# Optimization experiments

Measured on AMD Instinct MI355X. Metric: run time of the kernel, lower is better.

The kernel has to match this reference:

```python
import jax, jax.numpy as jnp
import numpy as np

E = 1024   # embed_dim
H = 16     # num_heads
R = 256    # rank
HD = E // H
B, S = 2, 2048


def setup_inputs() -> dict:
    key = jax.random.key(0)
    ks = jax.random.split(key, 20)
    sc = 0.02
    d = {
        'query': jax.random.normal(ks[0], (B, S, E), jnp.float32),
        'key':   jax.random.normal(ks[1], (B, S, E), jnp.float32),
        'value': jax.random.normal(ks[2], (B, S, E), jnp.float32),
    }
    names = ['q', 'k', 'v', 'o']
    i = 3
    for n in names:
        d[f'W{n}_lo'] = jax.random.normal(ks[i], (E, R), jnp.float32) * sc; i += 1
        d[f'b{n}_lo'] = jnp.zeros((R,), jnp.float32)
        d[f'W{n}_hi'] = jax.random.normal(ks[i], (R, E), jnp.float32) * sc; i += 1
        d[f'b{n}_hi'] = jnp.zeros((E,), jnp.float32)
    return d


def _lowrank(x, W_lo, b_lo, W_hi, b_hi):
    # Linear(E->R) then Linear(R->E)
    return (x @ W_lo + b_lo) @ W_hi + b_hi


def reference(query, key, value,
              Wq_lo, bq_lo, Wq_hi, bq_hi,
              Wk_lo, bk_lo, Wk_hi, bk_hi,
              Wv_lo, bv_lo, Wv_hi, bv_hi,
              Wo_lo, bo_lo, Wo_hi, bo_hi):
    b, s, _ = query.shape
    q = _lowrank(query, Wq_lo, bq_lo, Wq_hi, bq_hi)
    k = _lowrank(key,   Wk_lo, bk_lo, Wk_hi, bk_hi)
    v = _lowrank(value, Wv_lo, bv_lo, Wv_hi, bv_hi)
    # (B, S, E) -> (B, H, S, HD)
    q = q.reshape(b, s, H, HD).transpose(0, 2, 1, 3)
    k = k.reshape(b, s, H, HD).transpose(0, 2, 1, 3)
    v = v.reshape(b, s, H, HD).transpose(0, 2, 1, 3)
    scores = jnp.einsum('bhqd,bhkd->bhqk', q, k) / jnp.sqrt(jnp.float32(HD))
    attn = jax.nn.softmax(scores, axis=-1)  # dropout p=0.0 -> identity
    out = jnp.einsum('bhqk,bhkd->bhqd', attn, v)
    out = out.transpose(0, 2, 1, 3).reshape(b, s, E)
    return _lowrank(out, Wo_lo, bo_lo, Wo_hi, bo_hi)
```

## Files before the change

kernel.cpp:

```cpp
#include <hip/hip_runtime.h>

namespace {

constexpr int kE  = 1024;
constexpr int kH  = 16;
constexpr int kR  = 256;
constexpr int kHD = 64;
constexpr int kB  = 2;
constexpr int kS  = 2048;
constexpr int kM  = kB * kS;

typedef float  floatx4 __attribute__((ext_vector_type(4)));
typedef short  short8  __attribute__((ext_vector_type(8)));
typedef short  short4  __attribute__((ext_vector_type(4)));
typedef unsigned int uint2v __attribute__((ext_vector_type(2)));

__device__ inline short f2bf(float f) {
  union { float f; unsigned u; } x{f};
  unsigned r = x.u + 0x7FFF + ((x.u >> 16) & 1);
  return (short)(r >> 16);
}

__device__ inline unsigned cvt_pk_bf16(float a, float b) {
#if defined(__HIP_DEVICE_COMPILE__)
  unsigned r;
  asm("v_cvt_pk_bf16_f32 %0, %1, %2" : "=v"(r) : "v"(a), "v"(b));
  return r;
#else
  return (unsigned)(unsigned short)f2bf(a) | ((unsigned)(unsigned short)f2bf(b) << 16);
#endif
}

__device__ inline short4 pack2(unsigned a, unsigned b) {
  union { uint2v u; short4 s; } x;
  x.u[0] = a; x.u[1] = b;
  return x.s;
}

__device__ inline short8 pack4(unsigned a, unsigned b, unsigned c, unsigned d) {
  union { unsigned u[4]; short8 s; } x;
  x.u[0] = a; x.u[1] = b; x.u[2] = c; x.u[3] = d;
  return x.s;
}

__device__ inline float fexp2(float x) {
#if defined(__HIP_DEVICE_COMPILE__) && __has_builtin(__builtin_amdgcn_exp2f)
  return __builtin_amdgcn_exp2f(x);
#else
  return exp2f(x);
#endif
}

__device__ inline int xcd_swz256(int bid) {
  return ((bid & 7) << 5) | (bid >> 3);
}

#if defined(__HIP_DEVICE_COMPILE__)
  #if __has_builtin(__builtin_amdgcn_mfma_f32_16x16x16bf16_1k)
    #define MFMA16(a, b, c) __builtin_amdgcn_mfma_f32_16x16x16bf16_1k(a, b, c, 0, 0, 0)
  #elif __has_builtin(__builtin_amdgcn_mfma_f32_16x16x16_bf16)
    #define MFMA16(a, b, c) __builtin_amdgcn_mfma_f32_16x16x16_bf16(a, b, c, 0, 0, 0)
  #else
    #error "no 16x16x16 bf16 MFMA builtin on device"
  #endif
#else
  #define MFMA16(a, b, c) (c)
#endif

struct PrepArgs { const float* src[8]; short* dst[8]; };

__global__ __launch_bounds__(256) void prep_weights(PrepArgs pa) {
  const int id = blockIdx.y;
  const bool lo = (id & 1) == 0;
  const int K = lo ? 1024 : 256;
  const int N = lo ? 256 : 1024;
  const int tiles_k = K >> 6;
  const int k0 = (blockIdx.x % tiles_k) * 64;
  const int n0 = (blockIdx.x / tiles_k) * 64;
  const float* src = pa.src[id];
  short* dst = pa.dst[id];

  __shared__ float tile[64][68];
  const int t  = threadIdx.x;
  const int c4 = (t & 15) * 4;
  const int r  = t >> 4;

#pragma unroll
  for (int i = 0; i < 4; ++i) {
    const int rk = r + i * 16;
    *(float4*)&tile[rk][c4] = *(const float4*)&src[(size_t)(k0 + rk) * N + n0 + c4];
  }
  __syncthreads();
#pragma unroll
  for (int i = 0; i < 4; ++i) {
    const int rn = r + i * 16;
    short4 o = { f2bf(tile[c4 + 0][rn]), f2bf(tile[c4 + 1][rn]),
                 f2bf(tile[c4 + 2][rn]), f2bf(tile[c4 + 3][rn]) };
    *(short4*)&dst[(size_t)(n0 + rn) * K + k0 + c4] = o;
  }
}

struct GemmArgs {
  const short* A[3]; const short* Bt[3]; const float* bias[3];
  void* C[3]; float scale[3];
};

template <int M, int N, int K, int BM, int BN, int MODE>
__global__ __launch_bounds__(256) void gemm_bf16(GemmArgs args) {
  constexpr int TILES_N = N / BN;
  constexpr int WTM = BM / 2, WTN = BN / 2;
  constexpr int FI = WTM / 16, FJ = WTN / 16;
  constexpr int AROUNDS = (BM * 64) / 4096;
  constexpr int BROUNDS = (BN * 64) / 4096;
  constexpr int P = 80;
  static_assert((M / BM) * (N / BN) == 256, "swizzle assumes nwg=256");
  static_assert(MODE != 1 || M == kM, "MODE1 decode assumes M=4096");

  const int z = blockIdx.y;
  const int swz = xcd_swz256(blockIdx.x);
  const int row0 = (swz / TILES_N) * BM;
  const int col0 = (swz % TILES_N) * BN;
  const short* A  = args.A[z];
  const short* Bt = args.Bt[z];
  const float* bias = args.bias[z];
  const float scale = args.scale[z];

  __shared__ short As[BM * 40];
  __shared__ short Bs[BN * 40];

  const int t    = threadIdx.x;
  const int wave = t >> 6;
  const int lane = t & 63;
  const int lq   = lane & 15;
  const int quad = lane >> 4;
  const int wm0  = (wave >> 1) * WTM;
  const int wn0  = (wave & 1) * WTN;

  const int srow = t >> 2;
  const int scol = (t & 3) * 8;
  const int sbyte = (t & 3) * 16;

  floatx4 acc[FI][FJ] = {};

  short8 ra[AROUNDS], rb[BROUNDS];
#pragma unroll
  for (int r = 0; r < AROUNDS; ++r)
    ra[r] = *(const short8*)(A + (size_t)(row0 + r * 64 + srow) * K + scol);
#pragma unroll
  for (int r = 0; r < BROUNDS; ++r)
    rb[r] = *(const short8*)(Bt + (size_t)(col0 + r * 64 + srow) * K + scol);

  for (int kk = 0; kk < K; kk += 32) {
    __syncthreads();
#pragma unroll
    for (int r = 0; r < AROUNDS; ++r)
      *(short8*)((char*)As + (r * 64 + srow) * P + sbyte) = ra[r];
#pragma unroll
    for (int r = 0; r < BROUNDS; ++r)
      *(short8*)((char*)Bs + (r * 64 + srow) * P + sbyte) = rb[r];
    __syncthreads();

    if (kk + 32 < K) {
#pragma unroll
      for (int r = 0; r < AROUNDS; ++r)
        ra[r] = *(const short8*)(A + (size_t)(row0 + r * 64 + srow) * K + kk + 32 + scol);
#pragma unroll
      for (int r = 0; r < BROUNDS; ++r)
        rb[r] = *(const short8*)(Bt + (size_t)(col0 + r * 64 + srow) * K + kk + 32 + scol);
    }

    short8 af[FI], bf[FJ];
#pragma unroll
    for (int i = 0; i < FI; ++i)
      af[i] = *(const short8*)((const char*)As + ((wm0 + i * 16 + lq) * P + quad * 16));
#pragma unroll
    for (int j = 0; j < FJ; ++j)
      bf[j] = *(const short8*)((const char*)Bs + ((wn0 + j * 16 + lq) * P + quad * 16));
#pragma unroll
    for (int i = 0; i < FI; ++i)
#pragma unroll
      for (int j = 0; j < FJ; ++j)
        acc[i][j] = __builtin_amdgcn_mfma_f32_16x16x32_bf16(af[i], bf[j], acc[i][j], 0, 0, 0);
  }

#pragma unroll
  for (int i = 0; i < FI; ++i) {
    const int rbase = row0 + wm0 + i * 16 + quad * 4;
#pragma unroll
    for (int j = 0; j < FJ; ++j) {
      const int col = col0 + wn0 + j * 16 + lq;
      const float bj = bias[col];
      if (MODE == 2) {
        float* C = (float*)args.C[z];
#pragma unroll
        for (int r = 0; r < 4; ++r)
          C[(size_t)(rbase + r) * N + col] = (acc[i][j][r] + bj) * scale;
      } else if (MODE == 1) {
        short* C = (short*)args.C[z];
        const int h = col >> 6, d = col & 63;
        const int b = rbase >> 11, s = rbase & 2047;
        if (z == 2) {
          short4 o = { f2bf(acc[i][j][0] + bj), f2bf(acc[i][j][1] + bj),
                       f2bf(acc[i][j][2] + bj), f2bf(acc[i][j][3] + bj) };
          *(short4*)&C[((size_t)((b * 16 + h) * 64 + d)) * 2048 + s] = o;
        } else {
#pragma unroll
          for (int r = 0; r < 4; ++r)
            C[((size_t)((b * 16 + h) * 2048 + s + r)) * 64 + d] =
                f2bf((acc[i][j][r] + bj) * scale);
        }
      } else {
        short* C = (short*)args.C[z];
#pragma unroll
        for (int r = 0; r < 4; ++r)
          C[(size_t)(rbase + r) * N + col] = f2bf((acc[i][j][r] + bj) * scale);
      }
    }
  }
}

struct GemmLoArgs {
  const float* A[3]; const short* Bt[3]; const float* bias[3]; short* C[3];
};

__global__ __launch_bounds__(256) void gemm_lo_f32a(GemmLoArgs args) {
  constexpr int N = kR, K = kE, BM = 64, BN = 64;
  constexpr int TILES_N = N / BN;
  constexpr int WTM = BM / 2, WTN = BN / 2;
  constexpr int FI = WTM / 16, FJ = WTN / 16;
  constexpr int P = 80;
  static_assert((kM / BM) * (N / BN) == 256, "swizzle assumes nwg=256");

  const int z = blockIdx.y;
  const int swz = xcd_swz256(blockIdx.x);
  const int row0 = (swz / TILES_N) * BM;
  const int col0 = (swz % TILES_N) * BN;
  const float* A  = args.A[z];
  const short* Bt = args.Bt[z];
  const float* bias = args.bias[z];
  short* C = args.C[z];

  __shared__ float As32[64][36];
  __shared__ short Bs[BN * 40];

  const int t    = threadIdx.x;
  const int wave = t >> 6;
  const int lane = t & 63;
  const int lq   = lane & 15;
  const int quad = lane >> 4;
  const int wm0  = (wave >> 1) * WTM;
  const int wn0  = (wave & 1) * WTN;

  const int arow  = t >> 2;
  const int acolf = (t & 3) * 8;
  const int srow  = t >> 2;
  const int scol  = (t & 3) * 8;
  const int sbyte = (t & 3) * 16;

  floatx4 acc[FI][FJ] = {};

  const float* arow_p = A + (size_t)(row0 + arow) * K + acolf;
  float4 ga0 = *(const float4*)(arow_p);
  float4 ga1 = *(const float4*)(arow_p + 4);
  short8 rb  = *(const short8*)(Bt + (size_t)(col0 + srow) * K + scol);

  for (int kk = 0; kk < K; kk += 32) {
    __syncthreads();
    *(float4*)&As32[arow][acolf]     = ga0;
    *(float4*)&As32[arow][acolf + 4] = ga1;
    *(short8*)((char*)Bs + srow * P + sbyte) = rb;
    __syncthreads();

    if (kk + 32 < K) {
      ga0 = *(const float4*)(arow_p + kk + 32);
      ga1 = *(const float4*)(arow_p + kk + 36);
      rb  = *(const short8*)(Bt + (size_t)(col0 + srow) * K + kk + 32 + scol);
    }

    short8 af[FI], bf[FJ];
#pragma unroll
    for (int i = 0; i < FI; ++i) {
      const int r = wm0 + i * 16 + lq;
      float4 f0 = *(const float4*)&As32[r][quad * 8];
      float4 f1 = *(const float4*)&As32[r][quad * 8 + 4];
      af[i] = pack4(cvt_pk_bf16(f0.x, f0.y), cvt_pk_bf16(f0.z, f0.w),
                    cvt_pk_bf16(f1.x, f1.y), cvt_pk_bf16(f1.z, f1.w));
    }
#pragma unroll
    for (int j = 0; j < FJ; ++j)
      bf[j] = *(const short8*)((const char*)Bs + ((wn0 + j * 16 + lq) * P + quad * 16));
#pragma unroll
    for (int i = 0; i < FI; ++i)
#pragma unroll
      for (int j = 0; j < FJ; ++j)
        acc[i][j] = __builtin_amdgcn_mfma_f32_16x16x32_bf16(af[i], bf[j], acc[i][j], 0, 0, 0);
  }

#pragma unroll
  for (int i = 0; i < FI; ++i) {
    const int rbase = row0 + wm0 + i * 16 + quad * 4;
#pragma unroll
    for (int j = 0; j < FJ; ++j) {
      const int col = col0 + wn0 + j * 16 + lq;
      const float bj = bias[col];
#pragma unroll
      for (int r = 0; r < 4; ++r)
        C[(size_t)(rbase + r) * N + col] = f2bf(acc[i][j][r] + bj);
    }
  }
}

__global__ __launch_bounds__(256) void attn_mfma(
    const short* __restrict__ Qp, const short* __restrict__ Kp,
    const short* __restrict__ Vtp, short* __restrict__ O)
{
  __shared__ short Ks[64][72];
  __shared__ short Vs[64][72];

  const int t    = threadIdx.x;
  const int wave = t >> 6;
  const int lane = t & 63;
  const int lq   = lane & 15;
  const int quad = lane >> 4;

  const int q0 = blockIdx.x * 128;
  const int bh = blockIdx.y;
  const int b  = bh >> 4;
  const int h  = bh & 15;

  short8 qf0[2], qf1[2];
#pragma unroll
  for (int qt = 0; qt < 2; ++qt) {
    const short* qrow = Qp + ((size_t)bh * kS + q0 + wave * 32 + qt * 16 + lq) * 64;
    qf0[qt] = *(const short8*)(qrow + quad * 8);
    qf1[qt] = *(const short8*)(qrow + 32 + quad * 8);
  }

  const short* Kbase = Kp  + (size_t)bh * kS * 64;
  const short* Vbase = Vtp + (size_t)bh * 64 * kS;

  const int srow = wave * 16 + (lane >> 3);
  const int scol = (lane & 7) * 8;

  floatx4 Oacc[4][2] = {};
  float m[2] = {-1e30f, -1e30f};
  float l[2] = {0.f, 0.f};

  short8 gk0 = *(const short8*)(Kbase + (size_t)(srow) * 64 + scol);
  short8 gk1 = *(const short8*)(Kbase + (size_t)(srow + 8) * 64 + scol);
  short8 gv0 = *(const short8*)(Vbase + (size_t)srow * kS + scol);
  short8 gv1 = *(const short8*)(Vbase + (size_t)(srow + 8) * kS + scol);

  for (int kc = 0; kc < kS; kc += 64) {
    __syncthreads();
    *(short8*)&Ks[srow][scol]     = gk0;
    *(short8*)&Ks[srow + 8][scol] = gk1;
    *(short8*)&Vs[srow][scol]     = gv0;
    *(short8*)&Vs[srow + 8][scol] = gv1;
    __syncthreads();

    if (kc + 64 < kS) {
      gk0 = *(const short8*)(Kbase + (size_t)(kc + 64 + srow) * 64 + scol);
      gk1 = *(const short8*)(Kbase + (size_t)(kc + 64 + srow + 8) * 64 + scol);
      gv0 = *(const short8*)(Vbase + (size_t)srow * kS + kc + 64 + scol);
      gv1 = *(const short8*)(Vbase + (size_t)(srow + 8) * kS + kc + 64 + scol);
    }

    floatx4 Sc[4][2];
#pragma unroll
    for (int tt = 0; tt < 4; ++tt) {
      short8 a0 = *(const short8*)&Ks[tt * 16 + lq][quad * 8];
      short8 a1 = *(const short8*)&Ks[tt * 16 + lq][32 + quad * 8];
#pragma unroll
      for (int qt = 0; qt < 2; ++qt) {
        floatx4 c = {};
        c = __builtin_amdgcn_mfma_f32_16x16x32_bf16(a0, qf0[qt], c, 0, 0, 0);
        c = __builtin_amdgcn_mfma_f32_16x16x32_bf16(a1, qf1[qt], c, 0, 0, 0);
        Sc[tt][qt] = c;
      }
    }

    short4 pf[4][2];
#pragma unroll
    for (int qt = 0; qt < 2; ++qt) {
      float x0 = fmaxf(fmaxf(Sc[0][qt][0], Sc[0][qt][1]), fmaxf(Sc[0][qt][2], Sc[0][qt][3]));
      float x1 = fmaxf(fmaxf(Sc[1][qt][0], Sc[1][qt][1]), fmaxf(Sc[1][qt][2], Sc[1][qt][3]));
      float x2 = fmaxf(fmaxf(Sc[2][qt][0], Sc[2][qt][1]), fmaxf(Sc[2][qt][2], Sc[2][qt][3]));
      float x3 = fmaxf(fmaxf(Sc[3][qt][0], Sc[3][qt][1]), fmaxf(Sc[3][qt][2], Sc[3][qt][3]));
      float plane = fmaxf(fmaxf(x0, x1), fmaxf(x2, x3));

      if (!__all(plane <= m[qt] + 10.f)) {
        float mc = fmaxf(plane, __shfl_xor(plane, 16, 64));
        mc = fmaxf(mc, __shfl_xor(mc, 32, 64));
        const float mn = fmaxf(m[qt], mc);
        const float a = fexp2(m[qt] - mn);
        m[qt] = mn;
        l[qt] *= a;
#pragma unroll
        for (int dt = 0; dt < 4; ++dt) Oacc[dt][qt] *= a;
      }

      float ls = 0.f;
#pragma unroll
      for (int tt = 0; tt < 4; ++tt) {
        float p0 = fexp2(Sc[tt][qt][0] - m[qt]);
        float p1 = fexp2(Sc[tt][qt][1] - m[qt]);
        float p2 = fexp2(Sc[tt][qt][2] - m[qt]);
        float p3 = fexp2(Sc[tt][qt][3] - m[qt]);
        ls += (p0 + p1) + (p2 + p3);
        pf[tt][qt] = pack2(cvt_pk_bf16(p0, p1), cvt_pk_bf16(p2, p3));
      }
      l[qt] += ls;
    }

#pragma unroll
    for (int dt = 0; dt < 4; ++dt) {
#pragma unroll
      for (int tt = 0; tt < 4; ++tt) {
        short4 vf = *(const short4*)&Vs[dt * 16 + lq][tt * 16 + quad * 4];
#pragma unroll
        for (int qt = 0; qt < 2; ++qt)
          Oacc[dt][qt] = MFMA16(vf, pf[tt][qt], Oacc[dt][qt]);
      }
    }
  }

#pragma unroll
  for (int qt = 0; qt < 2; ++qt) {
    float lv = l[qt];
    lv += __shfl_xor(lv, 16, 64);
    lv += __shfl_xor(lv, 32, 64);
    const float inv = 1.f / lv;

    short* orow = O + ((size_t)(b * kS + q0 + wave * 32 + qt * 16 + lq)) * kE + h * kHD;
#pragma unroll
    for (int dt = 0; dt < 4; ++dt) {
      short4 o = pack2(cvt_pk_bf16(Oacc[dt][qt][0] * inv, Oacc[dt][qt][1] * inv),
                       cvt_pk_bf16(Oacc[dt][qt][2] * inv, Oacc[dt][qt][3] * inv));
      *(short4*)&orow[dt * 16 + quad * 4] = o;
    }
  }
}

}

extern "C" void kernel_launch(void* const* d_in, const int* in_sizes, int n_in,
                              void* d_out, int out_size, void* d_ws, size_t ws_size,
                              hipStream_t stream) {
  short* ws = (short*)d_ws;
  short* Tq  = ws;
  short* Tk  = Tq  + (size_t)kM * kR;
  short* Tv  = Tk  + (size_t)kM * kR;
  short* Qh  = Tv  + (size_t)kM * kR;
  short* Kh  = Qh  + (size_t)kM * kE;
  short* Vth = Kh  + (size_t)kM * kE;
  short* Ab  = Vth + (size_t)kM * kE;
  short* To  = Ab  + (size_t)kM * kE;
  short* Wt  = To  + (size_t)kM * kR;

  short* WtArr[8];
  for (int i = 0; i < 8; ++i) WtArr[i] = Wt + (size_t)i * (kE * kR);

  PrepArgs pa;
  const int widx[8] = {3, 5, 7, 9, 11, 13, 15, 17};
  for (int i = 0; i < 8; ++i) { pa.src[i] = (const float*)d_in[widx[i]]; pa.dst[i] = WtArr[i]; }
  prep_weights<<<dim3(64, 8), dim3(256), 0, stream>>>(pa);

  {
    GemmLoArgs ga;
    ga.A[0] = (const float*)d_in[0]; ga.A[1] = (const float*)d_in[1]; ga.A[2] = (const float*)d_in[2];
    ga.Bt[0] = WtArr[0]; ga.Bt[1] = WtArr[2]; ga.Bt[2] = WtArr[4];
    ga.bias[0] = (const float*)d_in[4]; ga.bias[1] = (const float*)d_in[8]; ga.bias[2] = (const float*)d_in[12];
    ga.C[0] = Tq; ga.C[1] = Tk; ga.C[2] = Tv;
    gemm_lo_f32a<<<dim3(256, 3), dim3(256), 0, stream>>>(ga);
  }

  {
    GemmArgs ga;
    ga.A[0] = Tq; ga.A[1] = Tk; ga.A[2] = Tv;
    ga.Bt[0] = WtArr[1]; ga.Bt[1] = WtArr[3]; ga.Bt[2] = WtArr[5];
    ga.bias[0] = (const float*)d_in[6]; ga.bias[1] = (const float*)d_in[10]; ga.bias[2] = (const float*)d_in[14];
    ga.C[0] = Qh; ga.C[1] = Kh; ga.C[2] = Vth;
    ga.scale[0] = 0.125f * 1.44269504088896340736f;
    ga.scale[1] = 1.f; ga.scale[2] = 1.f;
    gemm_bf16<kM, kE, kR, 128, 128, 1><<<dim3(256, 3), dim3(256), 0, stream>>>(ga);
  }

  attn_mfma<<<dim3(kS / 128, kB * kH), dim3(256), 0, stream>>>(Qh, Kh, Vth, Ab);

  {
    GemmArgs ga;
    ga.A[0] = Ab; ga.Bt[0] = WtArr[6];
    ga.bias[0] = (const float*)d_in[16];
    ga.C[0] = To; ga.scale[0] = 1.f;
    gemm_bf16<kM, kR, kE, 64, 64, 0><<<dim3(256, 1), dim3(256), 0, stream>>>(ga);
  }
  {
    GemmArgs ga;
    ga.A[0] = To; ga.Bt[0] = WtArr[7];
    ga.bias[0] = (const float*)d_in[18];
    ga.C[0] = d_out; ga.scale[0] = 1.f;
    gemm_bf16<kM, kE, kR, 128, 128, 2><<<dim3(256, 1), dim3(256), 0, stream>>>(ga);
  }
}
```

Before: 243.8 us.

## Fuse output low-rank projections into one kernel keeping intermediate in LDS

Replaces the two output-projection GEMM launches with a single kernel. Each block computes a 64x256 low-rank intermediate from the attention output, keeps it in shared memory as bf16, then multiplies by the high-rank weight for its 256-column slice. This removes one launch and the global round trip of the intermediate. The cost is that the first GEMM is recomputed by each of the four column blocks that share a row tile.

```diff
diff --git a/kernel.cpp b/kernel.cpp
--- a/kernel.cpp
+++ b/kernel.cpp
@@ -310,6 +310,134 @@
   }
 }
 
+__global__ __launch_bounds__(256) void gemm_out_fused(
+    const short* __restrict__ Ab,
+    const short* __restrict__ BtLo,
+    const short* __restrict__ BtHi,
+    const float* __restrict__ bLo,
+    const float* __restrict__ bHi,
+    float* __restrict__ Out)
+{
+  constexpr int P  = 80;
+  constexpr int PT = 264;
+
+  const int swz = xcd_swz256(blockIdx.x);
+  const int r0 = (swz >> 2) * 64;
+  const int c0 = (swz & 3) * 256;
+
+  __shared__ short As[64 * 40];
+  __shared__ short Bs[256 * 40];
+  __shared__ short To[64 * PT];
+
+  const int t    = threadIdx.x;
+  const int wave = t >> 6;
+  const int lane = t & 63;
+  const int lq   = lane & 15;
+  const int quad = lane >> 4;
+  const int wm0  = (wave >> 1) * 32;
+  const int wn0  = (wave & 1) * 128;
+
+  const int srow  = t >> 2;
+  const int scol  = (t & 3) * 8;
+  const int sbyte = (t & 3) * 16;
+
+  floatx4 acc[2][8] = {};
+
+  short8 ra = *(const short8*)(Ab + (size_t)(r0 + srow) * 1024 + scol);
+  short8 rb[4];
+#pragma unroll
+  for (int r = 0; r < 4; ++r)
+    rb[r] = *(const short8*)(BtLo + (size_t)(r * 64 + srow) * 1024 + scol);
+
+  for (int kk = 0; kk < 1024; kk += 32) {
+    __syncthreads();
+    *(short8*)((char*)As + srow * P + sbyte) = ra;
+#pragma unroll
+    for (int r = 0; r < 4; ++r)
+      *(short8*)((char*)Bs + (r * 64 + srow) * P + sbyte) = rb[r];
+    __syncthreads();
+
+    if (kk + 32 < 1024) {
+      ra = *(const short8*)(Ab + (size_t)(r0 + srow) * 1024 + kk + 32 + scol);
+#pragma unroll
+      for (int r = 0; r < 4; ++r)
+        rb[r] = *(const short8*)(BtLo + (size_t)(r * 64 + srow) * 1024 + kk + 32 + scol);
+    }
+
+    short8 af[2], bf[8];
+#pragma unroll
+    for (int i = 0; i < 2; ++i)
+      af[i] = *(const short8*)((const char*)As + ((wm0 + i * 16 + lq) * P + quad * 16));
+#pragma unroll
+    for (int j = 0; j < 8; ++j)
+      bf[j] = *(const short8*)((const char*)Bs + ((wn0 + j * 16 + lq) * P + quad * 16));
+#pragma unroll
+    for (int i = 0; i < 2; ++i)
+#pragma unroll
+      for (int j = 0; j < 8; ++j)
+        acc[i][j] = __builtin_amdgcn_mfma_f32_16x16x32_bf16(af[i], bf[j], acc[i][j], 0, 0, 0);
+  }
+
+  short8 rb2[4];
+#pragma unroll
+  for (int r = 0; r < 4; ++r)
+    rb2[r] = *(const short8*)(BtHi + (size_t)(c0 + r * 64 + srow) * 256 + scol);
+
+#pragma unroll
+  for (int i = 0; i < 2; ++i) {
+    const int rbase = wm0 + i * 16 + quad * 4;
+#pragma unroll
+    for (int j = 0; j < 8; ++j) {
+      const int col = wn0 + j * 16 + lq;
+      const float bj = bLo[col];
+#pragma unroll
+      for (int r = 0; r < 4; ++r)
+        To[(rbase + r) * PT + col] = f2bf(acc[i][j][r] + bj);
+    }
+  }
+
+  floatx4 acc2[2][8] = {};
+  for (int kk = 0; kk < 256; kk += 32) {
+    __syncthreads();
+#pragma unroll
+    for (int r = 0; r < 4; ++r)
+      *(short8*)((char*)Bs + (r * 64 + srow) * P + sbyte) = rb2[r];
+    __syncthreads();
+
+    if (kk + 32 < 256) {
+#pragma unroll
+      for (int r = 0; r < 4; ++r)
+        rb2[r] = *(const short8*)(BtHi + (size_t)(c0 + r * 64 + srow) * 256 + kk + 32 + scol);
+    }
+
+    short8 af[2], bf[8];
+#pragma unroll
+    for (int i = 0; i < 2; ++i)
+      af[i] = *(const short8*)&To[(wm0 + i * 16 + lq) * PT + kk + quad * 8];
+#pragma unroll
+    for (int j = 0; j < 8; ++j)
+      bf[j] = *(const short8*)((const char*)Bs + ((wn0 + j * 16 + lq) * P + quad * 16));
+#pragma unroll
+    for (int i = 0; i < 2; ++i)
+#pragma unroll
+      for (int j = 0; j < 8; ++j)
+        acc2[i][j] = __builtin_amdgcn_mfma_f32_16x16x32_bf16(af[i], bf[j], acc2[i][j], 0, 0, 0);
+  }
+
+#pragma unroll
+  for (int i = 0; i < 2; ++i) {
+    const int rbase = r0 + wm0 + i * 16 + quad * 4;
+#pragma unroll
+    for (int j = 0; j < 8; ++j) {
+      const int col = c0 + wn0 + j * 16 + lq;
+      const float bj = bHi[col];
+#pragma unroll
+      for (int r = 0; r < 4; ++r)
+        Out[(size_t)(rbase + r) * 1024 + col] = acc2[i][j][r] + bj;
+    }
+  }
+}
+
 __global__ __launch_bounds__(256) void attn_mfma(
     const short* __restrict__ Qp, const short* __restrict__ Kp,
     const short* __restrict__ Vtp, short* __restrict__ O)
@@ -455,8 +583,7 @@
   short* Kh  = Qh  + (size_t)kM * kE;
   short* Vth = Kh  + (size_t)kM * kE;
   short* Ab  = Vth + (size_t)kM * kE;
-  short* To  = Ab  + (size_t)kM * kE;
-  short* Wt  = To  + (size_t)kM * kR;
+  short* Wt  = Ab  + (size_t)kM * kE;
 
   short* WtArr[8];
   for (int i = 0; i < 8; ++i) WtArr[i] = Wt + (size_t)i * (kE * kR);
@@ -488,18 +615,7 @@
 
   attn_mfma<<<dim3(kS / 128, kB * kH), dim3(256), 0, stream>>>(Qh, Kh, Vth, Ab);
 
-  {
-    GemmArgs ga;
-    ga.A[0] = Ab; ga.Bt[0] = WtArr[6];
-    ga.bias[0] = (const float*)d_in[16];
-    ga.C[0] = To; ga.scale[0] = 1.f;
-    gemm_bf16<kM, kR, kE, 64, 64, 0><<<dim3(256, 1), dim3(256), 0, stream>>>(ga);
-  }
-  {
-    GemmArgs ga;
-    ga.A[0] = To; ga.Bt[0] = WtArr[7];
-    ga.bias[0] = (const float*)d_in[18];
-    ga.C[0] = d_out; ga.scale[0] = 1.f;
-    gemm_bf16<kM, kE, kR, 128, 128, 2><<<dim3(256, 1), dim3(256), 0, stream>>>(ga);
-  }
-}
+  gemm_out_fused<<<dim3(256), dim3(256), 0, stream>>>(
+      Ab, WtArr[6], WtArr[7],
+      (const float*)d_in[16], (const float*)d_in[18], (float*)d_out);
+}
```

After: 253.9 us. 1.04x slower.

## Double-buffer LDS tiles in both GEMM kernels to halve barriers

Applied to the files above, without the earlier changes.

Both bf16 GEMM kernels now use two LDS buffers and two register staging sets. Each iteration handles two 32-wide k-steps, prefetching two tiles ahead, and needs one barrier per k-step instead of two. The goal is to overlap global loads and LDS stores with MFMA work and cut synchronization overhead. The cost is twice the LDS and more registers, which can lower occupancy.

```diff
diff --git a/kernel.cpp b/kernel.cpp
--- a/kernel.cpp
+++ b/kernel.cpp
@@ -110,11 +110,13 @@
   constexpr int TILES_N = N / BN;
   constexpr int WTM = BM / 2, WTN = BN / 2;
   constexpr int FI = WTM / 16, FJ = WTN / 16;
-  constexpr int AROUNDS = (BM * 64) / 4096;
-  constexpr int BROUNDS = (BN * 64) / 4096;
+  constexpr int AROUNDS = BM / 64;
+  constexpr int BROUNDS = BN / 64;
   constexpr int P = 80;
-  static_assert((M / BM) * (N / BN) == 256, "swizzle assumes nwg=256");
+  constexpr int NWG = (M / BM) * (N / BN);
+  static_assert(NWG == 256, "swizzle assumes nwg=256");
   static_assert(MODE != 1 || M == kM, "MODE1 decode assumes M=4096");
+  static_assert(K % 64 == 0, "even k-tile count required");
 
   const int z = blockIdx.y;
   const int swz = xcd_swz256(blockIdx.x);
@@ -125,8 +127,8 @@
   const float* bias = args.bias[z];
   const float scale = args.scale[z];
 
-  __shared__ short As[BM * 40];
-  __shared__ short Bs[BN * 40];
+  __shared__ short As[2][BM * 40];
+  __shared__ short Bs[2][BN * 40];
 
   const int t    = threadIdx.x;
   const int wave = t >> 6;
@@ -141,46 +143,55 @@
   const int sbyte = (t & 3) * 16;
 
   floatx4 acc[FI][FJ] = {};
-
-  short8 ra[AROUNDS], rb[BROUNDS];
-#pragma unroll
-  for (int r = 0; r < AROUNDS; ++r)
-    ra[r] = *(const short8*)(A + (size_t)(row0 + r * 64 + srow) * K + scol);
-#pragma unroll
-  for (int r = 0; r < BROUNDS; ++r)
-    rb[r] = *(const short8*)(Bt + (size_t)(col0 + r * 64 + srow) * K + scol);
-
-  for (int kk = 0; kk < K; kk += 32) {
-    __syncthreads();
+  short8 saA[AROUNDS], saB[BROUNDS], sbA[AROUNDS], sbB[BROUNDS];
+
+  auto load_t = [&](short8* aA, short8* aB, int kk) {
 #pragma unroll
     for (int r = 0; r < AROUNDS; ++r)
-      *(short8*)((char*)As + (r * 64 + srow) * P + sbyte) = ra[r];
+      aA[r] = *(const short8*)(A + (size_t)(row0 + r * 64 + srow) * K + kk + scol);
 #pragma unroll
     for (int r = 0; r < BROUNDS; ++r)
-      *(short8*)((char*)Bs + (r * 64 + srow) * P + sbyte) = rb[r];
-    __syncthreads();
-
-    if (kk + 32 < K) {
-#pragma unroll
-      for (int r = 0; r < AROUNDS; ++r)
-        ra[r] = *(const short8*)(A + (size_t)(row0 + r * 64 + srow) * K + kk + 32 + scol);
-#pragma unroll
-      for (int r = 0; r < BROUNDS; ++r)
-        rb[r] = *(const short8*)(Bt + (size_t)(col0 + r * 64 + srow) * K + kk + 32 + scol);
-    }
-
+      aB[r] = *(const short8*)(Bt + (size_t)(col0 + r * 64 + srow) * K + kk + scol);
+  };
+  auto store_t = [&](const short8* aA, const short8* aB, int b) {
+#pragma unroll
+    for (int r = 0; r < AROUNDS; ++r)
+      *(short8*)((char*)As[b] + (r * 64 + srow) * P + sbyte) = aA[r];
+#pragma unroll
+    for (int r = 0; r < BROUNDS; ++r)
+      *(short8*)((char*)Bs[b] + (r * 64 + srow) * P + sbyte) = aB[r];
+  };
+  auto mma = [&](int b) {
     short8 af[FI], bf[FJ];
 #pragma unroll
     for (int i = 0; i < FI; ++i)
-      af[i] = *(const short8*)((const char*)As + ((wm0 + i * 16 + lq) * P + quad * 16));
+      af[i] = *(const short8*)((const char*)As[b] + ((wm0 + i * 16 + lq) * P + quad * 16));
 #pragma unroll
     for (int j = 0; j < FJ; ++j)
-      bf[j] = *(const short8*)((const char*)Bs + ((wn0 + j * 16 + lq) * P + quad * 16));
+      bf[j] = *(const short8*)((const char*)Bs[b] + ((wn0 + j * 16 + lq) * P + quad * 16));
 #pragma unroll
     for (int i = 0; i < FI; ++i)
 #pragma unroll
       for (int j = 0; j < FJ; ++j)
         acc[i][j] = __builtin_amdgcn_mfma_f32_16x16x32_bf16(af[i], bf[j], acc[i][j], 0, 0, 0);
+  };
+
+  load_t(saA, saB, 0);
+  store_t(saA, saB, 0);
+  load_t(saA, saB, 32);
+  __syncthreads();
+
+  for (int k0 = 0; k0 < K; k0 += 64) {
+    if (k0 + 64 < K) load_t(sbA, sbB, k0 + 64);
+    mma(0);
+    store_t(saA, saB, 1);
+    __syncthreads();
+    if (k0 + 96 < K) load_t(saA, saB, k0 + 96);
+    mma(1);
+    if (k0 + 64 < K) {
+      store_t(sbA, sbB, 0);
+      __syncthreads();
+    }
   }
 
 #pragma unroll
@@ -229,6 +240,7 @@
   constexpr int WTM = BM / 2, WTN = BN / 2;
   constexpr int FI = WTM / 16, FJ = WTN / 16;
   constexpr int P = 80;
+  constexpr int PA = 36;
   static_assert((kM / BM) * (N / BN) == 256, "swizzle assumes nwg=256");
 
   const int z = blockIdx.y;
@@ -240,8 +252,8 @@
   const float* bias = args.bias[z];
   short* C = args.C[z];
 
-  __shared__ float As32[64][36];
-  __shared__ short Bs[BN * 40];
+  __shared__ float As32[2][64 * PA];
+  __shared__ short Bs[2][BN * 40];
 
   const int t    = threadIdx.x;
   const int wave = t >> 6;
@@ -258,42 +270,57 @@
   const int sbyte = (t & 3) * 16;
 
   floatx4 acc[FI][FJ] = {};
-
   const float* arow_p = A + (size_t)(row0 + arow) * K + acolf;
-  float4 ga0 = *(const float4*)(arow_p);
-  float4 ga1 = *(const float4*)(arow_p + 4);
-  short8 rb  = *(const short8*)(Bt + (size_t)(col0 + srow) * K + scol);
-
-  for (int kk = 0; kk < K; kk += 32) {
-    __syncthreads();
-    *(float4*)&As32[arow][acolf]     = ga0;
-    *(float4*)&As32[arow][acolf + 4] = ga1;
-    *(short8*)((char*)Bs + srow * P + sbyte) = rb;
-    __syncthreads();
-
-    if (kk + 32 < K) {
-      ga0 = *(const float4*)(arow_p + kk + 32);
-      ga1 = *(const float4*)(arow_p + kk + 36);
-      rb  = *(const short8*)(Bt + (size_t)(col0 + srow) * K + kk + 32 + scol);
-    }
-
+
+  float4 saG0, saG1, sbG0, sbG1;
+  short8 saR, sbR;
+
+  auto load_t = [&](float4& g0, float4& g1, short8& rbv, int kk) {
+    g0  = *(const float4*)(arow_p + kk);
+    g1  = *(const float4*)(arow_p + kk + 4);
+    rbv = *(const short8*)(Bt + (size_t)(col0 + srow) * K + kk + scol);
+  };
+  auto store_t = [&](const float4& g0, const float4& g1, const short8& rbv, int b) {
+    *(float4*)&As32[b][arow * PA + acolf]     = g0;
+    *(float4*)&As32[b][arow * PA + acolf + 4] = g1;
+    *(short8*)((char*)Bs[b] + srow * P + sbyte) = rbv;
+  };
+  auto mma = [&](int b) {
     short8 af[FI], bf[FJ];
 #pragma unroll
     for (int i = 0; i < FI; ++i) {
       const int r = wm0 + i * 16 + lq;
-      float4 f0 = *(const float4*)&As32[r][quad * 8];
-      float4 f1 = *(const float4*)&As32[r][quad * 8 + 4];
+      float4 f0 = *(const float4*)&As32[b][r * PA + quad * 8];
+      float4 f1 = *(const float4*)&As32[b][r * PA + quad * 8 + 4];
       af[i] = pack4(cvt_pk_bf16(f0.x, f0.y), cvt_pk_bf16(f0.z, f0.w),
                     cvt_pk_bf16(f1.x, f1.y), cvt_pk_bf16(f1.z, f1.w));
     }
 #pragma unroll
     for (int j = 0; j < FJ; ++j)
-      bf[j] = *(const short8*)((const char*)Bs + ((wn0 + j * 16 + lq) * P + quad * 16));
+      bf[j] = *(const short8*)((const char*)Bs[b] + ((wn0 + j * 16 + lq) * P + quad * 16));
 #pragma unroll
     for (int i = 0; i < FI; ++i)
 #pragma unroll
       for (int j = 0; j < FJ; ++j)
         acc[i][j] = __builtin_amdgcn_mfma_f32_16x16x32_bf16(af[i], bf[j], acc[i][j], 0, 0, 0);
+  };
+
+  load_t(saG0, saG1, saR, 0);
+  store_t(saG0, saG1, saR, 0);
+  load_t(saG0, saG1, saR, 32);
+  __syncthreads();
+
+  for (int k0 = 0; k0 < K; k0 += 64) {
+    if (k0 + 64 < K) load_t(sbG0, sbG1, sbR, k0 + 64);
+    mma(0);
+    store_t(saG0, saG1, saR, 1);
+    __syncthreads();
+    if (k0 + 96 < K) load_t(saG0, saG1, saR, k0 + 96);
+    mma(1);
+    if (k0 + 64 < K) {
+      store_t(sbG0, sbG1, sbR, 0);
+      __syncthreads();
+    }
   }
 
 #pragma unroll
```

New measurement: 244.2 us. No clear change (+0.2%).
